# Kernel tuning notes

Measured on AMD Instinct MI355X. Metric: run time of the kernel, lower is better.

Reference implementation:

```python
import jax, jax.numpy as jnp
import numpy as np

B, H, I = 16384, 512, 256
EPS = 1e-8

def setup_inputs() -> dict:
    key = jax.random.key(0)
    ks = jax.random.split(key, 10)
    x = jax.random.normal(ks[0], (B, I), dtype=jnp.float32)
    hx_re = jax.random.normal(ks[1], (B, H), dtype=jnp.float32) * 0.05
    hx_im = jax.random.normal(ks[2], (B, H), dtype=jnp.float32) * 0.05
    # diag = exp(1j * U(-pi, pi)) -> store angles as real params
    diag_angles = jax.random.uniform(ks[3], (3 * H,), dtype=jnp.float32,
                                     minval=-np.pi, maxval=np.pi)
    # rotation = U(0,1)*2 - (1+1j): real part in [-1,1], imag part in [-1,1]
    rot_re = jax.random.uniform(ks[4], (2 * H,), dtype=jnp.float32) * 2.0 - 1.0
    rot_im = jax.random.uniform(ks[5], (2 * H,), dtype=jnp.float32) * 2.0 - 1.0
    # xavier-scale complex Linear weight (hidden, input), no bias
    w_scale = float(np.sqrt(2.0 / (I + H)))
    W_re = jax.random.normal(ks[6], (H, I), dtype=jnp.float32) * w_scale
    W_im = jax.random.normal(ks[7], (H, I), dtype=jnp.float32) * w_scale
    beta = jnp.zeros((H,), dtype=jnp.float32)  # ModReLU bias, zeros init
    perm = jax.random.permutation(ks[8], H).astype(jnp.int32)
    return {"x": x, "hx_re": hx_re, "hx_im": hx_im,
            "diag_angles": diag_angles, "rot_re": rot_re, "rot_im": rot_im,
            "W_re": W_re, "W_im": W_im, "beta": beta, "perm": perm}

def _unit(v):
    # complex_unit_norm: v / (||v|| + eps), norm over last dim
    return v / (jnp.linalg.norm(v) + EPS)

def _apply_householder(h, v):
    # h @ (I - 2 v v^H) == h - 2 (h @ v) v^H  (rank-1 form, no NxN matrix)
    return h - 2.0 * (h @ v)[:, None] * jnp.conj(v)[None, :]

def reference(x, hx_re, hx_im, diag_angles, rot_re, rot_im, W_re, W_im, beta, perm):
    diag = jnp.exp(1j * diag_angles)                 # complex64, |.| = 1
    d1, d2, d3 = jnp.split(diag, 3)
    rot = rot_re + 1j * rot_im
    r1, r2 = jnp.split(rot, 2)
    v1 = _unit(r1)
    v2 = _unit(r2)

    h = hx_re + 1j * hx_im                           # (B, H) complex64
    h = jnp.fft.fft(d1[None, :] * h, axis=-1)        # D1 then F
    h = _apply_householder(h, v1)                    # R1
    h = jnp.fft.ifft(d2[None, :] * h[:, perm], axis=-1)  # Pi, D2, F^-1
    h = d3[None, :] * _apply_householder(h, v2)      # R2 then D3
    # complex Linear on real input: x @ W^T with complex W
    emb = (x @ W_re.T) + 1j * (x @ W_im.T)
    h = h + emb
    # ModReLU: relu(|z| + beta) * exp(1j * angle(z))
    mag = jnp.abs(h)
    out = jax.nn.relu(mag + beta[None, :]) * jnp.exp(1j * jnp.angle(h))
    # return as real (B, H, 2) [real, imag] for real-valued harness
    return jnp.stack([out.real, out.imag], axis=-1)
```

## Files before the change

### kernel.cpp

```cpp
#include <hip/hip_runtime.h>
#include <hip/hip_bf16.h>
#include <stdint.h>
#include <stddef.h>

typedef __bf16 bf16;
typedef bf16 bf16x8 __attribute__((ext_vector_type(8)));
typedef float f32x4 __attribute__((ext_vector_type(4)));

#define EPSN 1e-8f
#define TWO_PI 6.283185307179586f

#define NB 16384
#define NH 512
#define NI 256
#define KTOT 1280
#define NKT 20

__device__ __forceinline__ float2 cmul(float2 a, float2 b) {
  return make_float2(a.x * b.x - a.y * b.y, a.x * b.y + a.y * b.x);
}
__device__ __forceinline__ float2 cmulconj(float2 a, float2 b) {
  return make_float2(a.x * b.x + a.y * b.y, a.y * b.x - a.x * b.y);
}
__device__ __forceinline__ float2 cadd(float2 a, float2 b) {
  return make_float2(a.x + b.x, a.y + b.y);
}
__device__ __forceinline__ int brev9(int i) {
  return (int)(__brev((unsigned)i) >> 23);
}

__device__ __forceinline__ void gload16(const bf16* g, bf16* l) {
  __builtin_amdgcn_global_load_lds(
      (const __attribute__((address_space(1))) void*)g,
      (__attribute__((address_space(3))) void*)l, 16, 0, 0);
}

__global__ __launch_bounds__(256) void prep(
    const float* __restrict__ ang, const float* __restrict__ rre,
    const float* __restrict__ rim, const float* __restrict__ wre,
    const float* __restrict__ wim, const int* __restrict__ perm,
    const float* __restrict__ hxre, const float* __restrict__ hxim,
    const float* __restrict__ x, bf16* __restrict__ Bm,
    bf16* __restrict__ Apack) {
  __shared__ float2 bufA[512];
  __shared__ float2 bufB[512];
  __shared__ float2 redw[4];
  __shared__ float2 bc;
  __shared__ float2 red2[256];

  const int bid = blockIdx.x;
  const int t = threadIdx.x;

  if (bid >= 512) {
    const int tid = (bid - 512) * 256 + t;
    const int b = tid / 160;
    const int o = tid - b * 160;
    const float* src;
    if (o < 64)
      src = hxre + (size_t)b * 512 + o * 8;
    else if (o < 128)
      src = hxim + (size_t)b * 512 + (o - 64) * 8;
    else
      src = x + (size_t)b * 256 + (o - 128) * 8;
    float4 f0 = ((const float4*)src)[0];
    float4 f1 = ((const float4*)src)[1];
    bf16x8 v;
    v[0] = (bf16)f0.x; v[1] = (bf16)f0.y; v[2] = (bf16)f0.z; v[3] = (bf16)f0.w;
    v[4] = (bf16)f1.x; v[5] = (bf16)f1.y; v[6] = (bf16)f1.z; v[7] = (bf16)f1.w;
    *(bf16x8*)(Apack + (size_t)b * KTOT + o * 8) = v;
    return;
  }

  const int j = bid;
  const int j0 = t, j1 = t + 256;

  const float r1x0 = rre[j0], r1y0 = rim[j0];
  const float r1x1 = rre[j1], r1y1 = rim[j1];
  const float r2x0 = rre[512 + j0], r2y0 = rim[512 + j0];
  const float r2x1 = rre[512 + j1], r2y1 = rim[512 + j1];
  red2[t] = make_float2(r1x0 * r1x0 + r1y0 * r1y0 + r1x1 * r1x1 + r1y1 * r1y1,
                        r2x0 * r2x0 + r2y0 * r2y0 + r2x1 * r2x1 + r2y1 * r2y1);
  __syncthreads();
  for (int off = 128; off > 0; off >>= 1) {
    if (t < off) {
      red2[t].x += red2[t + off].x;
      red2[t].y += red2[t + off].y;
    }
    __syncthreads();
  }
  const float inv1 = 1.0f / (sqrtf(red2[0].x) + EPSN);
  const float inv2 = 1.0f / (sqrtf(red2[0].y) + EPSN);
  const float2 v1a = make_float2(r1x0 * inv1, r1y0 * inv1);
  const float2 v1b = make_float2(r1x1 * inv1, r1y1 * inv1);
  const float2 v2a = make_float2(r2x0 * inv2, r2y0 * inv2);
  const float2 v2b = make_float2(r2x1 * inv2, r2y1 * inv2);

  {
    float sj, cj;
    __sincosf(ang[j], &sj, &cj);
    const float2 dj = make_float2(cj, sj);
    float2 z = make_float2(0.f, 0.f);
    bufA[brev9(j0)] = (j0 == j) ? dj : z;
    bufA[brev9(j1)] = (j1 == j) ? dj : z;
  }
  __syncthreads();

#pragma unroll
  for (int st = 0; st < 9; ++st) {
    const int half = 1 << st;
    const int pos = t & (half - 1);
    const int i0 = ((t >> st) << (st + 1)) + pos;
    const int i1 = i0 + half;
    const float angv = -TWO_PI * (float)pos / (float)(2 << st);
    float sn, cs;
    __sincosf(angv, &sn, &cs);
    float2 u = bufA[i0];
    float2 w = bufA[i1];
    float2 tw = make_float2(cs * w.x - sn * w.y, cs * w.y + sn * w.x);
    bufA[i0] = make_float2(u.x + tw.x, u.y + tw.y);
    bufA[i1] = make_float2(u.x - tw.x, u.y - tw.y);
    __syncthreads();
  }

  {
    float2 p = cadd(cmul(bufA[j0], v1a), cmul(bufA[j1], v1b));
    for (int off = 32; off > 0; off >>= 1) {
      p.x += __shfl_down(p.x, off);
      p.y += __shfl_down(p.y, off);
    }
    if ((t & 63) == 0) redw[t >> 6] = p;
    __syncthreads();
    if (t == 0) bc = cadd(cadd(redw[0], redw[1]), cadd(redw[2], redw[3]));
    __syncthreads();
  }
  const float2 dot1 = bc;

  {
    float2 c0 = cmulconj(dot1, v1a);
    float2 c1 = cmulconj(dot1, v1b);
    float2 a0 = bufA[j0], a1 = bufA[j1];
    bufA[j0] = make_float2(a0.x - 2.f * c0.x, a0.y - 2.f * c0.y);
    bufA[j1] = make_float2(a1.x - 2.f * c1.x, a1.y - 2.f * c1.y);
  }
  __syncthreads();

  {
    int p0 = perm[j0], p1 = perm[j1];
    float s0, c0, s1, c1;
    __sincosf(ang[512 + j0], &s0, &c0);
    __sincosf(ang[512 + j1], &s1, &c1);
    float2 g0 = cmul(make_float2(c0, s0), bufA[p0]);
    float2 g1 = cmul(make_float2(c1, s1), bufA[p1]);
    bufB[brev9(j0)] = g0;
    bufB[brev9(j1)] = g1;
  }
  __syncthreads();

#pragma unroll
  for (int st = 0; st < 9; ++st) {
    const int half = 1 << st;
    const int pos = t & (half - 1);
    const int i0 = ((t >> st) << (st + 1)) + pos;
    const int i1 = i0 + half;
    const float angv = TWO_PI * (float)pos / (float)(2 << st);
    float sn, cs;
    __sincosf(angv, &sn, &cs);
    float2 u = bufB[i0];
    float2 w = bufB[i1];
    float2 tw = make_float2(cs * w.x - sn * w.y, cs * w.y + sn * w.x);
    bufB[i0] = make_float2(u.x + tw.x, u.y + tw.y);
    bufB[i1] = make_float2(u.x - tw.x, u.y - tw.y);
    __syncthreads();
  }

  {
    float2 q = cadd(cmul(bufB[j0], v2a), cmul(bufB[j1], v2b));
    for (int off = 32; off > 0; off >>= 1) {
      q.x += __shfl_down(q.x, off);
      q.y += __shfl_down(q.y, off);
    }
    if ((t & 63) == 0) redw[t >> 6] = q;
    __syncthreads();
    if (t == 0) bc = cadd(cadd(redw[0], redw[1]), cadd(redw[2], redw[3]));
    __syncthreads();
  }
  const float invN = 1.0f / 512.0f;
  const float2 dot2 = make_float2(bc.x * invN, bc.y * invN);

#pragma unroll
  for (int e = 0; e < 2; ++e) {
    const int i = (e == 0) ? j0 : j1;
    const float2 vj = (e == 0) ? v2a : v2b;
    float2 h2 = make_float2(bufB[i].x * invN, bufB[i].y * invN);
    float2 c2 = cmulconj(dot2, vj);
    float2 hh = make_float2(h2.x - 2.f * c2.x, h2.y - 2.f * c2.y);
    float s3, c3;
    __sincosf(ang[1024 + i], &s3, &c3);
    float2 u = cmul(make_float2(c3, s3), hh);
    bf16* r0 = Bm + (size_t)(2 * i) * KTOT;
    bf16* r1 = Bm + (size_t)(2 * i + 1) * KTOT;
    r0[j] = (bf16)u.x;
    r0[512 + j] = (bf16)(-u.y);
    r1[j] = (bf16)u.y;
    r1[512 + j] = (bf16)u.x;
  }

  Bm[(size_t)(2 * j) * KTOT + 1024 + t] = (bf16)wre[j * NI + t];
  Bm[(size_t)(2 * j + 1) * KTOT + 1024 + t] = (bf16)wim[j * NI + t];
}


#define BARM() __builtin_amdgcn_s_barrier()
#define WVM(n) asm volatile("s_waitcnt vmcnt(" #n ")" ::: "memory")

__device__ __forceinline__ void stA(const bf16* gA, bf16* Asb, int wv, int h,
                                    int kt) {
  const int r0 = h * 64 + wv * 8;
  const int r1 = r0 + 128;
  gload16(gA + (size_t)r0 * KTOT + kt * 64, Asb + r0 * 64);
  gload16(gA + (size_t)r1 * KTOT + kt * 64, Asb + r1 * 64);
}
__device__ __forceinline__ void stB(const bf16* gB, bf16* Bsb, int wv, int h,
                                    int kt) {
  const int u0 = wv * 2, u1 = u0 + 1;
  const int r0 = (u0 >> 2) * 64 + h * 32 + (u0 & 3) * 8;
  const int r1 = (u1 >> 2) * 64 + h * 32 + (u1 & 3) * 8;
  gload16(gB + (size_t)r0 * KTOT + kt * 64, Bsb + r0 * 64);
  gload16(gB + (size_t)r1 * KTOT + kt * 64, Bsb + r1 * 64);
}

__device__ __forceinline__ void lda(const bf16* Asb, int rowbase,
                                    const int (&co)[2], bf16x8 (&af)[4][2]) {
#pragma unroll
  for (int mi = 0; mi < 4; ++mi)
#pragma unroll
    for (int kh = 0; kh < 2; ++kh)
      af[mi][kh] = *(const bf16x8*)&Asb[(rowbase + mi * 16) * 64 + co[kh]];
}
__device__ __forceinline__ void ldb(const bf16* Bsb, int rowbase,
                                    const int (&co)[2], bf16x8 (&bb)[2][2]) {
#pragma unroll
  for (int ni = 0; ni < 2; ++ni)
#pragma unroll
    for (int kh = 0; kh < 2; ++kh)
      bb[ni][kh] = *(const bf16x8*)&Bsb[(rowbase + ni * 16) * 64 + co[kh]];
}
__device__ __forceinline__ void mmq(const bf16x8 (&af)[4][2],
                                    const bf16x8 (&bb)[2][2],
                                    f32x4 (&acc)[8][4], int mh, int nh) {
  __builtin_amdgcn_s_setprio(1);
#pragma unroll
  for (int mi = 0; mi < 4; ++mi)
#pragma unroll
    for (int ni = 0; ni < 2; ++ni)
#pragma unroll
      for (int kh = 0; kh < 2; ++kh)
        acc[mh * 4 + mi][nh * 2 + ni] = __builtin_amdgcn_mfma_f32_16x16x32_bf16(
            af[mi][kh], bb[ni][kh], acc[mh * 4 + mi][nh * 2 + ni], 0, 0, 0);
  __builtin_amdgcn_s_setprio(0);
}

__global__ __launch_bounds__(512, 2) void gemm_fused(
    const bf16* __restrict__ Apack, const bf16* __restrict__ Bm,
    const float* __restrict__ beta, float* __restrict__ out) {
  __shared__ bf16 As[2][256 * 64];
  __shared__ bf16 Bs[2][256 * 64];

  const int t = threadIdx.x;
  const int lane = t & 63;
  const int wv = t >> 6;

  const int id = blockIdx.x;
  const int xcd = id & 7;
  const int lix = id >> 3;
  const int mBase = (xcd * 8 + (lix >> 2)) * 256;
  const int nBase = (lix & 3) * 256;

  const int sub = lane >> 3;
  const int chunk = (lane & 7) ^ sub;
  const bf16* gA = Apack + (size_t)(mBase + sub) * KTOT + chunk * 8;
  const bf16* gB = Bm + (size_t)(nBase + sub) * KTOT + chunk * 8;

  const int lr = lane & 15;
  const int lq = lane >> 4;
  const int lrm = lr & 7;
  const int waveM = wv & 1;
  const int waveN = wv >> 1;

  const int co[2] = {(lq ^ lrm) * 8, ((4 + lq) ^ lrm) * 8};
  const int arow = waveM * 128 + lr;
  const int brow = waveN * 64 + lr;

  f32x4 acc[8][4] = {};
  bf16x8 af[4][2], b0[2][2], b1[2][2];

  stA(gA, &As[0][0], wv, 0, 0);
  stB(gB, &Bs[0][0], wv, 0, 0);
  stA(gA, &As[0][0], wv, 1, 0);
  stB(gB, &Bs[0][0], wv, 1, 0);
  stA(gA, &As[1][0], wv, 0, 1);
  stB(gB, &Bs[1][0], wv, 0, 1);
  WVM(4);
  BARM();

  for (int i = 0; i < 10; ++i) {
    const int t1 = 2 * i + 1;
    const int t2 = (t1 + 1 < NKT) ? t1 + 1 : NKT - 1;
    const int t3 = (t1 + 2 < NKT) ? t1 + 2 : NKT - 1;

    lda(&As[0][0], arow, co, af);
    ldb(&Bs[0][0], brow, co, b0);
    stA(gA, &As[1][0], wv, 1, t1);
    BARM();
    mmq(af, b0, acc, 0, 0);
    BARM();
    ldb(&Bs[0][0], brow + 32, co, b1);
    stB(gB, &Bs[1][0], wv, 1, t1);
    BARM();
    mmq(af, b1, acc, 0, 1);
    BARM();
    lda(&As[0][0], arow + 64, co, af);
    stA(gA, &As[0][0], wv, 0, t2);
    BARM();
    mmq(af, b0, acc, 1, 0);
    BARM();
    stB(gB, &Bs[0][0], wv, 0, t2);
    BARM();
    mmq(af, b1, acc, 1, 1);
    WVM(4);
    BARM();

    lda(&As[1][0], arow, co, af);
    ldb(&Bs[1][0], brow, co, b0);
    stA(gA, &As[0][0], wv, 1, t2);
    BARM();
    mmq(af, b0, acc, 0, 0);
    BARM();
    ldb(&Bs[1][0], brow + 32, co, b1);
    stB(gB, &Bs[0][0], wv, 1, t2);
    BARM();
    mmq(af, b1, acc, 0, 1);
    BARM();
    lda(&As[1][0], arow + 64, co, af);
    stA(gA, &As[1][0], wv, 0, t3);
    BARM();
    mmq(af, b0, acc, 1, 0);
    BARM();
    stB(gB, &Bs[1][0], wv, 0, t3);
    BARM();
    mmq(af, b1, acc, 1, 1);
    WVM(4);
    BARM();
  }
  WVM(0);

  const int col = lane & 15;
  const int row0 = lq * 4;
  const int parity = lane & 1;
#pragma unroll
  for (int nq = 0; nq < 4; ++nq) {
    const int n = nBase + waveN * 64 + nq * 16 + col;
    const float bet = beta[n >> 1];
#pragma unroll
    for (int mq = 0; mq < 8; ++mq) {
      const int mrow = mBase + waveM * 128 + mq * 16 + row0;
#pragma unroll
      for (int r = 0; r < 4; ++r) {
        float a = acc[mq][nq][r];
        float o = __shfl_xor(a, 1);
        float re = parity ? o : a;
        float im = parity ? a : o;
        float mag2 = re * re + im * im;
        float val;
        if (mag2 > 0.f) {
          float rs = __frsqrt_rn(mag2);
          float s = mag2 * rs + bet;
          val = (s > 0.f) ? (parity ? im : re) * (s * rs) : 0.f;
        } else {
          val = (bet > 0.f && parity == 0) ? bet : 0.f;
        }
        out[(size_t)(mrow + r) * 1024 + n] = val;
      }
    }
  }
}

extern "C" void kernel_launch(void* const* d_in, const int* in_sizes, int n_in,
                              void* d_out, int out_size, void* d_ws,
                              size_t ws_size, hipStream_t stream) {
  const float* x = (const float*)d_in[0];
  const float* hxre = (const float*)d_in[1];
  const float* hxim = (const float*)d_in[2];
  const float* ang = (const float*)d_in[3];
  const float* rre = (const float*)d_in[4];
  const float* rim = (const float*)d_in[5];
  const float* wre = (const float*)d_in[6];
  const float* wim = (const float*)d_in[7];
  const float* beta = (const float*)d_in[8];
  const int* perm = (const int*)d_in[9];

  char* ws = (char*)d_ws;
  bf16* Bm = (bf16*)ws;
  bf16* Apack = (bf16*)(ws + (size_t)1024 * KTOT * 2);

  prep<<<512 + (NB * 160) / 256, 256, 0, stream>>>(ang, rre, rim, wre, wim,
                                                   perm, hxre, hxim, x, Bm,
                                                   Apack);
  gemm_fused<<<256, 512, 0, stream>>>(Apack, Bm, beta, (float*)d_out);
}
```

Before: 200.8 us.

## Software-pipeline GEMM main loop, halving barriers and overlapping LDS reads with MFMA

Restructures the fused GEMM main loop so each MFMA quadrant is issued back-to-back with the LDS reads and global-to-LDS stores for the next step. The first fragment loads are peeled into a prologue and rotated to the end of each iteration. Roughly half of the block barriers are removed, and the MFMA loop is reordered to iterate over the K half on the outside. The aim is to cut barrier stalls and hide LDS latency behind matrix work, but it risks LDS read/write races and higher register pressure. In the last iteration it also issues loads and stores for clamped tile indices that are not needed.

```diff
diff --git a/kernel.cpp b/kernel.cpp
--- a/kernel.cpp
+++ b/kernel.cpp
@@ -250,11 +250,11 @@
                                     f32x4 (&acc)[8][4], int mh, int nh) {
   __builtin_amdgcn_s_setprio(1);
 #pragma unroll
-  for (int mi = 0; mi < 4; ++mi)
-#pragma unroll
-    for (int ni = 0; ni < 2; ++ni)
-#pragma unroll
-      for (int kh = 0; kh < 2; ++kh)
+  for (int kh = 0; kh < 2; ++kh)
+#pragma unroll
+    for (int mi = 0; mi < 4; ++mi)
+#pragma unroll
+      for (int ni = 0; ni < 2; ++ni)
         acc[mh * 4 + mi][nh * 2 + ni] = __builtin_amdgcn_mfma_f32_16x16x32_bf16(
             af[mi][kh], bb[ni][kh], acc[mh * 4 + mi][nh * 2 + ni], 0, 0, 0);
   __builtin_amdgcn_s_setprio(0);
@@ -294,62 +294,62 @@
   f32x4 acc[8][4] = {};
   bf16x8 af[4][2], b0[2][2], b1[2][2];
 
-  stA(gA, &As[0][0], wv, 0, 0);
-  stB(gB, &Bs[0][0], wv, 0, 0);
-  stA(gA, &As[0][0], wv, 1, 0);
-  stB(gB, &Bs[0][0], wv, 1, 0);
-  stA(gA, &As[1][0], wv, 0, 1);
-  stB(gB, &Bs[1][0], wv, 0, 1);
+  bf16* As0 = &As[0][0];
+  bf16* As1 = &As[1][0];
+  bf16* Bs0 = &Bs[0][0];
+  bf16* Bs1 = &Bs[1][0];
+
+  stA(gA, As0, wv, 0, 0);
+  stB(gB, Bs0, wv, 0, 0);
+  stA(gA, As0, wv, 1, 0);
+  stB(gB, Bs0, wv, 1, 0);
+  stA(gA, As1, wv, 0, 1);
+  stB(gB, Bs1, wv, 0, 1);
   WVM(4);
   BARM();
+  lda(As0, arow, co, af);
+  ldb(Bs0, brow, co, b0);
+  stA(gA, As1, wv, 1, 1);
+  BARM();
 
   for (int i = 0; i < 10; ++i) {
-    const int t1 = 2 * i + 1;
-    const int t2 = (t1 + 1 < NKT) ? t1 + 1 : NKT - 1;
-    const int t3 = (t1 + 2 < NKT) ? t1 + 2 : NKT - 1;
-
-    lda(&As[0][0], arow, co, af);
-    ldb(&Bs[0][0], brow, co, b0);
-    stA(gA, &As[1][0], wv, 1, t1);
-    BARM();
+    const int T1 = 2 * i + 1;
+    const int t2 = (T1 + 1 < NKT) ? T1 + 1 : NKT - 1;
+    const int t3 = (T1 + 2 < NKT) ? T1 + 2 : NKT - 1;
+
     mmq(af, b0, acc, 0, 0);
-    BARM();
-    ldb(&Bs[0][0], brow + 32, co, b1);
-    stB(gB, &Bs[1][0], wv, 1, t1);
+    ldb(Bs0, brow + 32, co, b1);
+    stB(gB, Bs1, wv, 1, T1);
     BARM();
     mmq(af, b1, acc, 0, 1);
-    BARM();
-    lda(&As[0][0], arow + 64, co, af);
-    stA(gA, &As[0][0], wv, 0, t2);
+    lda(As0, arow + 64, co, af);
+    stA(gA, As0, wv, 0, t2);
     BARM();
     mmq(af, b0, acc, 1, 0);
-    BARM();
-    stB(gB, &Bs[0][0], wv, 0, t2);
+    stB(gB, Bs0, wv, 0, t2);
+    WVM(4);
     BARM();
     mmq(af, b1, acc, 1, 1);
+    lda(As1, arow, co, af);
+    ldb(Bs1, brow, co, b0);
+    stA(gA, As0, wv, 1, t2);
+    BARM();
+    mmq(af, b0, acc, 0, 0);
+    ldb(Bs1, brow + 32, co, b1);
+    stB(gB, Bs0, wv, 1, t2);
+    BARM();
+    mmq(af, b1, acc, 0, 1);
+    lda(As1, arow + 64, co, af);
+    stA(gA, As1, wv, 0, t3);
+    BARM();
+    mmq(af, b0, acc, 1, 0);
+    stB(gB, Bs1, wv, 0, t3);
     WVM(4);
     BARM();
-
-    lda(&As[1][0], arow, co, af);
-    ldb(&Bs[1][0], brow, co, b0);
-    stA(gA, &As[0][0], wv, 1, t2);
-    BARM();
-    mmq(af, b0, acc, 0, 0);
-    BARM();
-    ldb(&Bs[1][0], brow + 32, co, b1);
-    stB(gB, &Bs[0][0], wv, 1, t2);
-    BARM();
-    mmq(af, b1, acc, 0, 1);
-    BARM();
-    lda(&As[1][0], arow + 64, co, af);
-    stA(gA, &As[1][0], wv, 0, t3);
-    BARM();
-    mmq(af, b0, acc, 1, 0);
-    BARM();
-    stB(gB, &Bs[1][0], wv, 0, t3);
-    BARM();
     mmq(af, b1, acc, 1, 1);
-    WVM(4);
+    lda(As0, arow, co, af);
+    ldb(Bs0, brow, co, b0);
+    stA(gA, As1, wv, 1, t3);
     BARM();
   }
   WVM(0);
```

Result: no change. 201.3 us (+0.2%).
